# Optimization experiments

Measured on AMD Instinct MI355X. Metric: run time of the kernel, lower is better.

The kernel has to match this reference:

```python
import jax, jax.numpy as jnp
import numpy as np

H, TH, NH, NL, NB = 512, 768, 8, 12, 2
NE, NU, NI, NNZ, K, B = 16000, 2000, 4000, 40000, 10, 64
MD = H // 2
GAMA = 0.1


def _prelu(x, a):
    return jnp.where(x >= 0, x, a * x)


def _spmm(r, c, v, X, n):
    # sparse [n, m] @ X: gather X rows by col index, scale, segment-sum by row.
    return jax.ops.segment_sum(v[:, None] * X[c], r, num_segments=n)


def _forward(systemid, adj_row, adj_col, itemid_set,
             token_embeds, adj_val, node_embeds, user_embedding,
             token_proj_w, token_proj_b, trans_w, trans_b, trans_t_w, trans_t_b,
             meta_w1, meta_b1, meta_w2, meta_b2, sim_w1, sim_w2,
             p1_w1, p1_b1, p1_w2, p1_b2, p2_w, p2_b, prelu_a):
    tok = token_embeds @ token_proj_w + token_proj_b               # [B, H]
    # grouped mean over rows sharing the same system id (vectorized segment-mean)
    same = (systemid[:, None] == systemid[None, :]).astype(tok.dtype)
    group_mean = (same @ tok) / same.sum(1, keepdims=True)         # [B, H]
    filt = _prelu(group_mean @ trans_w + trans_b, prelu_a) * group_mean
    h = jax.nn.relu(filt @ meta_w1 + meta_b1)
    mapping = (h @ meta_w2 + meta_b2).reshape(B, H, H)             # per-sample hypernet weights
    enhanced = jnp.einsum('bh,bhk->bk', user_embedding[systemid], mapping)
    all_tok = user_embedding.at[systemid].set(enhanced)            # [NU, H]
    tok_edge = jnp.zeros_like(user_embedding).at[systemid].set(group_mean)
    # similarity between (enhanced) user/token reps and item reps
    u_rep = all_tok @ sim_w1
    i_rep = node_embeds[itemid_set] @ sim_w2
    u_n = u_rep / jnp.maximum(jnp.linalg.norm(u_rep, axis=1, keepdims=True), 1e-12)
    i_n = i_rep / jnp.maximum(jnp.linalg.norm(i_rep, axis=1, keepdims=True), 1e-12)
    sim = jax.nn.sigmoid(u_n @ i_n.T)                              # [NU, NI]
    tv, ti = jax.lax.top_k(sim, K)
    # combined sparse adjacency = original COO + per-user top-k added edges
    rows = jnp.concatenate([adj_row, jnp.repeat(jnp.arange(NU), K)])
    cols = jnp.concatenate([adj_col, itemid_set[ti].reshape(-1)])
    vals = jnp.concatenate([adj_val, tv.reshape(-1)])
    v_u = vals / jax.ops.segment_sum(vals, rows, num_segments=NU)[rows]   # row-normalized user->item
    v_i = vals / jax.ops.segment_sum(vals, cols, num_segments=NE)[cols]   # row-normalized item->user
    # LightGCN-style 2-layer propagation with multiplicative token gating
    user_tok = _prelu(tok_edge @ trans_t_w + trans_t_b, prelu_a) * tok_edge
    u0, i0 = all_tok, node_embeds
    Ai0 = _spmm(rows, cols, v_u, i0, NU)
    u1 = Ai0 + Ai0 * user_tok
    Att = _spmm(cols, rows, v_i, user_tok, NE)
    i1 = _spmm(cols, rows, v_i, u0, NE) + Att * i0
    Ai1 = _spmm(rows, cols, v_u, i1, NU)
    u2 = Ai1 + Ai1 * user_tok
    i2 = _spmm(cols, rows, v_i, u1, NE) + Att * i1
    user_final = (u0 + u1 + u2) / 3.0
    item_final = (i0 + i1 + i2) / 3.0
    # reconstruction loss vs dense adjacency restricted to item columns
    inv = jnp.full((NE,), -1, jnp.int32).at[itemid_set].set(jnp.arange(NI, dtype=jnp.int32))
    icol = inv[adj_col]
    valid = (icol >= 0).astype(sim.dtype)
    dense = jnp.zeros((NU, NI), sim.dtype).at[adj_row, jnp.maximum(icol, 0)].add(adj_val * valid)
    loss = GAMA * jnp.mean((sim - dense) ** 2)
    # prefix-prompt projection from per-batch system embeddings
    sys_final = user_final[systemid][:, None, :]                   # [B, 1, H]
    p1 = jax.nn.relu(sys_final @ p1_w1 + p1_b1) @ p1_w2 + p1_b2 + sys_final
    p2 = p1 @ p2_w + p2_b
    prompt = p2.reshape(B, 1, NL, NB, NH, H // NH).transpose(2, 3, 0, 4, 1, 5)
    return prompt, item_final, loss


def setup_inputs():
    ks = jax.random.split(jax.random.key(0), 20)
    rng = np.random.default_rng(0)
    s = 0.02
    itemid_set = jnp.asarray(np.sort(rng.choice(NE, NI, replace=False)).astype(np.int32))
    user_embedding = (s * jax.random.normal(ks[4], (NU, H), jnp.float32)).at[0].set(0.0)
    return {
        'systemid': jax.random.randint(ks[0], (B,), 0, NU),
        'adj_row': jax.random.randint(ks[1], (NNZ,), 0, NU),
        'adj_col': jax.random.randint(ks[2], (NNZ,), 0, NE),
        'itemid_set': itemid_set,
        'token_embeds': jax.random.normal(ks[3], (B, TH), jnp.float32),
        'adj_val': jnp.ones((NNZ,), jnp.float32),
        'node_embeds': s * jax.random.normal(ks[5], (NE, H), jnp.float32),
        'user_embedding': user_embedding,
        'token_proj_w': s * jax.random.normal(ks[6], (TH, H), jnp.float32),
        'token_proj_b': jnp.zeros((H,), jnp.float32),
        'trans_w': s * jax.random.normal(ks[7], (H, H), jnp.float32),
        'trans_b': jnp.zeros((H,), jnp.float32),
        'trans_t_w': s * jax.random.normal(ks[8], (H, H), jnp.float32),
        'trans_t_b': jnp.zeros((H,), jnp.float32),
        'meta_w1': s * jax.random.normal(ks[9], (H, MD), jnp.float32),
        'meta_b1': jnp.zeros((MD,), jnp.float32),
        'meta_w2': s * jax.random.normal(ks[10], (MD, H * H), jnp.float32),
        'meta_b2': jnp.zeros((H * H,), jnp.float32),
        'sim_w1': jax.random.normal(ks[11], (H, H), jnp.float32),
        'sim_w2': jax.random.normal(ks[12], (H, H), jnp.float32),
        'p1_w1': s * jax.random.normal(ks[13], (H, MD), jnp.float32),
        'p1_b1': jnp.zeros((MD,), jnp.float32),
        'p1_w2': s * jax.random.normal(ks[14], (MD, H), jnp.float32),
        'p1_b2': jnp.zeros((H,), jnp.float32),
        'p2_w': s * jax.random.normal(ks[15], (H, NL * NB * H), jnp.float32),
        'p2_b': jnp.zeros((NL * NB * H,), jnp.float32),
        'prelu_a': jnp.array(0.25, jnp.float32),
    }


def reference(systemid, adj_row, adj_col, itemid_set, token_embeds, adj_val,
              node_embeds, user_embedding, token_proj_w, token_proj_b,
              trans_w, trans_b, trans_t_w, trans_t_b,
              meta_w1, meta_b1, meta_w2, meta_b2, sim_w1, sim_w2,
              p1_w1, p1_b1, p1_w2, p1_b2, p2_w, p2_b, prelu_a):
    return _forward(systemid, adj_row, adj_col, itemid_set, token_embeds, adj_val,
                    node_embeds, user_embedding, token_proj_w, token_proj_b,
                    trans_w, trans_b, trans_t_w, trans_t_b,
                    meta_w1, meta_b1, meta_w2, meta_b2, sim_w1, sim_w2,
                    p1_w1, p1_b1, p1_w2, p1_b2, p2_w, p2_b, prelu_a)
```

## Files before the change

### kernel.cpp

```cpp
#include <hip/hip_runtime.h>

#define H     512
#define THD   768
#define MDIM  256
#define NE    16000
#define NU    2000
#define NI    4000
#define NNZ   40000
#define KTOP  10
#define NBATCH 64
#define NEDGE 60000
#define GAMA  0.1f
#define P2N   12288
#define PROMPT_N 786432
#define NLOSSB 2048

__device__ __forceinline__ float sigmoidf(float x){ return 1.0f/(1.0f+expf(-x)); }
__device__ __forceinline__ float4 f4z(){ return make_float4(0.f,0.f,0.f,0.f); }

__device__ __forceinline__ void gll16(const float* g, float* l){
  __builtin_amdgcn_global_load_lds(
      (const __attribute__((address_space(1))) void*)g,
      (__attribute__((address_space(3))) void*)l, 16, 0, 0);
}

__global__ void k_tok(const float* __restrict__ A, const float* __restrict__ W,
                      const float* __restrict__ bias, float* __restrict__ C){
  int b=blockIdx.x, c=blockIdx.y*256+threadIdx.x;
  const float* a=A+b*THD; float s=bias[c];
  for(int k=0;k<THD;k++) s+=a[k]*W[k*H+c];
  C[b*H+c]=s;
}

__global__ void k_gm(const int* __restrict__ sysid, const float* __restrict__ tok,
                     float* __restrict__ gm){
  int b=blockIdx.x, c=blockIdx.y*256+threadIdx.x;
  int sid=sysid[b]; float s=0.f, cnt=0.f;
  for(int j=0;j<NBATCH;j++){ if(sysid[j]==sid){ s+=tok[j*H+c]; cnt+=1.f; } }
  gm[b*H+c]=s/cnt;
}

__global__ __launch_bounds__(512) void k_front(const int* __restrict__ sysid,
        const float* __restrict__ gm,
        const float* __restrict__ trans_w, const float* __restrict__ trans_b,
        const float* __restrict__ mw1, const float* __restrict__ mb1,
        const float* __restrict__ ue, const float* __restrict__ mb2,
        const float* __restrict__ trt_w, const float* __restrict__ trt_b,
        const float* __restrict__ pa,
        float* __restrict__ hh, float* __restrict__ ueT, float* __restrict__ enh,
        float* __restrict__ usertok){
  __shared__ float fl[512];
  __shared__ float hp[512];
  int b=blockIdx.x, t=threadIdx.x, which=blockIdx.y;
  if(which==0){
    const float* g=gm+b*H;
    float s=trans_b[t];
    for(int k=0;k<H;k++) s+=g[k]*trans_w[k*H+t];
    float al=pa[0]; float pr=(s>=0.f)? s : al*s;
    fl[t]=pr*g[t];
    __syncthreads();
    int m=t&255, half=t>>8;
    float s2=0.f; int k0=half*256;
    for(int k=0;k<256;k++) s2+=fl[k0+k]*mw1[(k0+k)*MDIM+m];
    hp[t]=s2;
    __syncthreads();
    if(t<256) hh[b*MDIM+t]=fmaxf(hp[t]+hp[t+256]+mb1[t],0.f);
  } else if(which==1){
    const float* u=ue+(size_t)sysid[b]*H;
    float v=u[t];
    ueT[t*64+b]=v;
    float s=0.f;
    for(int h=0;h<H;h++) s+=u[h]*mb2[(size_t)h*H+t];
    enh[b*H+t]=s;
  } else {
    const float* a=gm+b*H; float s=trt_b[t];
    for(int k=0;k<H;k++) s+=a[k]*trt_w[k*H+t];
    float al=pa[0]; float pr=(s>=0.f)? s : al*s;
    usertok[(size_t)sysid[b]*H+t]=pr*gm[b*H+t];
  }
}

#define HCH 8
__global__ __launch_bounds__(128) void k_big(const float* __restrict__ hh,
        const float* __restrict__ ueT, const float* __restrict__ w2,
        float* __restrict__ partials){
  __shared__ float a_lds[2][HCH][64];
  __shared__ float w_lds[2][HCH][256];
  int m=blockIdx.x;
  int kt=blockIdx.y&1, hs=blockIdx.y>>1;
  int k0=kt*256;
  int hbase=hs*256;
  int t=threadIdx.x;
  int kg=t&15, bg=t>>4;
  const float* w2m = w2 + (size_t)m*(size_t)(H*H);

  float4 acc[8][4];
  #pragma unroll
  for(int r=0;r<8;r++){
    #pragma unroll
    for(int c=0;c<4;c++) acc[r][c]=f4z();
  }

  #define STAGE(buf,hc) do{                                             \
    int h0=hbase+(hc)*HCH;                                              \
    gll16(ueT + (size_t)(h0+(t>>4))*64 + (t&15)*4,                      \
          &a_lds[buf][t>>4][(t&15)*4]);                                 \
    _Pragma("unroll")                                                   \
    for(int j=0;j<4;j++){                                               \
      int i=t+j*128;                                                    \
      gll16(w2m + (size_t)(h0+(i>>6))*H + k0 + (i&63)*4,                \
            &w_lds[buf][i>>6][(i&63)*4]);                               \
    }                                                                   \
  }while(0)

  STAGE(0,0);
  int cur=0;
  for(int hc=0;hc<32;hc++){
    __syncthreads();
    if(hc<31) STAGE(cur^1,hc+1);
    #pragma unroll
    for(int hl=0;hl<HCH;hl++){
      float4 aL=*(const float4*)&a_lds[cur][hl][bg*4];
      float4 aH=*(const float4*)&a_lds[cur][hl][32+bg*4];
      float4 w0=*(const float4*)&w_lds[cur][hl][kg*4];
      float4 w1=*(const float4*)&w_lds[cur][hl][64+kg*4];
      float4 w2v=*(const float4*)&w_lds[cur][hl][128+kg*4];
      float4 w3=*(const float4*)&w_lds[cur][hl][192+kg*4];
      #define FMA4(ac,av,wv) ac.x+=(av)*wv.x; ac.y+=(av)*wv.y; ac.z+=(av)*wv.z; ac.w+=(av)*wv.w;
      #define ROWC(r,av) FMA4(acc[r][0],av,w0) FMA4(acc[r][1],av,w1) FMA4(acc[r][2],av,w2v) FMA4(acc[r][3],av,w3)
      ROWC(0,aL.x) ROWC(1,aL.y) ROWC(2,aL.z) ROWC(3,aL.w)
      ROWC(4,aH.x) ROWC(5,aH.y) ROWC(6,aH.z) ROWC(7,aH.w)
      #undef ROWC
      #undef FMA4
    }
    cur^=1;
  }
  int slice=hs*256+m;
  #pragma unroll
  for(int r=0;r<8;r++){
    int br=(r<4)? (bg*4+r) : (32+bg*4+(r-4));
    float hv=hh[br*MDIM+m];
    float* p=partials+((size_t)slice*NBATCH+br)*H+k0+kg*4;
    *(float4*)(p)    =make_float4(acc[r][0].x*hv,acc[r][0].y*hv,acc[r][0].z*hv,acc[r][0].w*hv);
    *(float4*)(p+64) =make_float4(acc[r][1].x*hv,acc[r][1].y*hv,acc[r][1].z*hv,acc[r][1].w*hv);
    *(float4*)(p+128)=make_float4(acc[r][2].x*hv,acc[r][2].y*hv,acc[r][2].z*hv,acc[r][2].w*hv);
    *(float4*)(p+192)=make_float4(acc[r][3].x*hv,acc[r][3].y*hv,acc[r][3].z*hv,acc[r][3].w*hv);
  }
  #undef STAGE
}

__global__ void k_red1(const float* __restrict__ partials, float* __restrict__ partial2){
  int idx=blockIdx.x*256+threadIdx.x;
  int g=idx>>15, col=idx&32767;
  const float* p=partials+(size_t)g*16*32768+col;
  float s=0.f;
  #pragma unroll
  for(int m=0;m<16;m++) s+=p[(size_t)m*32768];
  partial2[idx]=s;
}
__global__ void k_red2s(const int* __restrict__ sysid, const float* __restrict__ partial2,
                        const float* __restrict__ enh, float* __restrict__ alltok){
  int idx=blockIdx.x*256+threadIdx.x;
  int b=idx>>9, k=idx&511;
  float s=enh[idx];
  #pragma unroll
  for(int g=0;g<32;g++) s+=partial2[(size_t)g*32768+idx];
  alltok[(size_t)sysid[b]*H+k]=s;
}

template<int EPI, bool NT, bool AIDX>
__device__ __forceinline__ void gemm_body(float (*As)[68], float (*Bs)[68],
        const float* __restrict__ A, const float* __restrict__ Bm,
        const float* __restrict__ bias, const int* __restrict__ aidx,
        float* __restrict__ C, int M, int N, int K, int bx, int by){
  int n0=bx*64, m0=by*64;
  int t=threadIdx.x;
  int tn=t&15, tm=t>>4;
  float4 pa[2], pb[2];
  #pragma unroll
  for(int i=0;i<2;i++){
    int idx=t+i*256; int r=idx>>3, q=idx&7;
    int grow=m0+r;
    pa[i]=f4z();
    if(grow<M){
      const float* arow=A+(size_t)(AIDX? aidx[grow]:grow)*K;
      pa[i]=*(const float4*)(arow+q*4);
    }
  }
  #pragma unroll
  for(int i=0;i<2;i++){
    if(!NT){
      int idx=t+i*256; int r=idx>>4, q=idx&15;
      pb[i]=*(const float4*)(Bm+(size_t)r*N+n0+q*4);
    } else {
      int idx=t+i*256; int r=idx>>3, q=idx&7;
      int gn=n0+r;
      pb[i]=f4z();
      if(gn<N) pb[i]=*(const float4*)(Bm+(size_t)gn*K+q*4);
    }
  }
  float acc[4][4]={};
  for(int kt=0;kt<K;kt+=32){
    __syncthreads();
    #pragma unroll
    for(int i=0;i<2;i++){
      int idx=t+i*256; int r=idx>>3, q=idx&7;
      As[q*4+0][r]=pa[i].x; As[q*4+1][r]=pa[i].y; As[q*4+2][r]=pa[i].z; As[q*4+3][r]=pa[i].w;
    }
    #pragma unroll
    for(int i=0;i<2;i++){
      if(!NT){
        int idx=t+i*256; int r=idx>>4, q=idx&15;
        *(float4*)&Bs[r][q*4]=pb[i];
      } else {
        int idx=t+i*256; int r=idx>>3, q=idx&7;
        Bs[q*4+0][r]=pb[i].x; Bs[q*4+1][r]=pb[i].y; Bs[q*4+2][r]=pb[i].z; Bs[q*4+3][r]=pb[i].w;
      }
    }
    __syncthreads();
    if(kt+32<K){
      #pragma unroll
      for(int i=0;i<2;i++){
        int idx=t+i*256; int r=idx>>3, q=idx&7;
        int grow=m0+r;
        pa[i]=f4z();
        if(grow<M){
          const float* arow=A+(size_t)(AIDX? aidx[grow]:grow)*K;
          pa[i]=*(const float4*)(arow+kt+32+q*4);
        }
      }
      #pragma unroll
      for(int i=0;i<2;i++){
        if(!NT){
          int idx=t+i*256; int r=idx>>4, q=idx&15;
          pb[i]=*(const float4*)(Bm+(size_t)(kt+32+r)*N+n0+q*4);
        } else {
          int idx=t+i*256; int r=idx>>3, q=idx&7;
          int gn=n0+r;
          pb[i]=f4z();
          if(gn<N) pb[i]=*(const float4*)(Bm+(size_t)gn*K+kt+32+q*4);
        }
      }
    }
    #pragma unroll 8
    for(int k=0;k<32;k++){
      float4 a4=*(const float4*)&As[k][tm*4];
      float4 b4=*(const float4*)&Bs[k][tn*4];
      acc[0][0]+=a4.x*b4.x; acc[0][1]+=a4.x*b4.y; acc[0][2]+=a4.x*b4.z; acc[0][3]+=a4.x*b4.w;
      acc[1][0]+=a4.y*b4.x; acc[1][1]+=a4.y*b4.y; acc[1][2]+=a4.y*b4.z; acc[1][3]+=a4.y*b4.w;
      acc[2][0]+=a4.z*b4.x; acc[2][1]+=a4.z*b4.y; acc[2][2]+=a4.z*b4.z; acc[2][3]+=a4.z*b4.w;
      acc[3][0]+=a4.w*b4.x; acc[3][1]+=a4.w*b4.y; acc[3][2]+=a4.w*b4.z; acc[3][3]+=a4.w*b4.w;
    }
  }
  #pragma unroll
  for(int bi=0;bi<4;bi++){
    int row=m0+tm*4+bi; if(row>=M) continue;
    #pragma unroll
    for(int ki=0;ki<4;ki++){
      int col=n0+tn*4+ki; if(col>=N) continue;
      float v=acc[bi][ki];
      if(EPI==0){ if(bias) v+=bias[col]; }
      else { v=sigmoidf(v); }
      C[(size_t)row*N+col]=v;
    }
  }
}

template<int EPI, bool NT, bool AIDX>
__global__ __launch_bounds__(256) void k_gemm(const float* __restrict__ A,
        const float* __restrict__ Bm, const float* __restrict__ bias,
        const int* __restrict__ aidx, float* __restrict__ C, int M, int N, int K){
  __shared__ float As[32][68];
  __shared__ float Bs[32][68];
  gemm_body<EPI,NT,AIDX>(As,Bs,A,Bm,bias,aidx,C,M,N,K,blockIdx.x,blockIdx.y);
}

__global__ __launch_bounds__(256) void k_gemm_ui(const float* __restrict__ alltok,
        const float* __restrict__ node_emb, const float* __restrict__ sw1,
        const float* __restrict__ sw2, const int* __restrict__ itemid,
        float* __restrict__ urep, float* __restrict__ irep){
  __shared__ float As[32][68];
  __shared__ float Bs[32][68];
  if(blockIdx.y<32)
    gemm_body<0,false,false>(As,Bs,alltok,sw1,nullptr,nullptr,urep,NU,H,H,blockIdx.x,blockIdx.y);
  else
    gemm_body<0,false,true >(As,Bs,node_emb,sw2,nullptr,itemid,irep,NI,H,H,blockIdx.x,blockIdx.y-32);
}

__global__ __launch_bounds__(512) void k_gemm_sim(const float* __restrict__ A,
        const float* __restrict__ Bm, float* __restrict__ C, int M, int N){
  __shared__ float As[32][132];
  __shared__ float Bs[32][260];
  int n0=blockIdx.x*256, m0=blockIdx.y*128;
  int t=threadIdx.x;
  int tn=t&31, tm=t>>5;
  float4 pa[2], pb[4];
  #pragma unroll
  for(int i=0;i<2;i++){
    int idx=t+i*512; int r=idx>>3, q=idx&7;
    pa[i]=f4z();
    if(m0+r<M) pa[i]=*(const float4*)(A+(size_t)(m0+r)*H+q*4);
  }
  #pragma unroll
  for(int i=0;i<4;i++){
    int idx=t+i*512; int r=idx>>3, q=idx&7;
    pb[i]=f4z();
    if(n0+r<N) pb[i]=*(const float4*)(Bm+(size_t)(n0+r)*H+q*4);
  }
  float4 acc[8][2];
  #pragma unroll
  for(int r=0;r<8;r++){ acc[r][0]=f4z(); acc[r][1]=f4z(); }
  for(int kt=0;kt<H;kt+=32){
    __syncthreads();
    #pragma unroll
    for(int i=0;i<2;i++){
      int idx=t+i*512; int r=idx>>3, q=idx&7;
      As[q*4+0][r]=pa[i].x; As[q*4+1][r]=pa[i].y; As[q*4+2][r]=pa[i].z; As[q*4+3][r]=pa[i].w;
    }
    #pragma unroll
    for(int i=0;i<4;i++){
      int idx=t+i*512; int r=idx>>3, q=idx&7;
      Bs[q*4+0][r]=pb[i].x; Bs[q*4+1][r]=pb[i].y; Bs[q*4+2][r]=pb[i].z; Bs[q*4+3][r]=pb[i].w;
    }
    __syncthreads();
    if(kt+32<H){
      #pragma unroll
      for(int i=0;i<2;i++){
        int idx=t+i*512; int r=idx>>3, q=idx&7;
        pa[i]=f4z();
        if(m0+r<M) pa[i]=*(const float4*)(A+(size_t)(m0+r)*H+kt+32+q*4);
      }
      #pragma unroll
      for(int i=0;i<4;i++){
        int idx=t+i*512; int r=idx>>3, q=idx&7;
        pb[i]=f4z();
        if(n0+r<N) pb[i]=*(const float4*)(Bm+(size_t)(n0+r)*H+kt+32+q*4);
      }
    }
    #pragma unroll 8
    for(int k=0;k<32;k++){
      float4 a0=*(const float4*)&As[k][tm*4];
      float4 a1=*(const float4*)&As[k][64+tm*4];
      float4 b0=*(const float4*)&Bs[k][tn*4];
      float4 b1=*(const float4*)&Bs[k][128+tn*4];
      #define FMA4(ac,av,bv) ac.x+=(av)*bv.x; ac.y+=(av)*bv.y; ac.z+=(av)*bv.z; ac.w+=(av)*bv.w;
      #define ROW(r,av) FMA4(acc[r][0],av,b0) FMA4(acc[r][1],av,b1)
      ROW(0,a0.x) ROW(1,a0.y) ROW(2,a0.z) ROW(3,a0.w)
      ROW(4,a1.x) ROW(5,a1.y) ROW(6,a1.z) ROW(7,a1.w)
      #undef ROW
      #undef FMA4
    }
  }
  #pragma unroll
  for(int r=0;r<8;r++){
    int row=m0+((r<4)? (tm*4+r) : (64+tm*4+(r-4)));
    if(row>=M) continue;
    #pragma unroll
    for(int c=0;c<2;c++){
      int col0=n0+c*128+tn*4;
      float vv[4]={acc[r][c].x,acc[r][c].y,acc[r][c].z,acc[r][c].w};
      #pragma unroll
      for(int j=0;j<4;j++){
        int col=col0+j;
        if(col<N) C[(size_t)row*N+col]=sigmoidf(vv[j]);
      }
    }
  }
}

__global__ __launch_bounds__(256) void k_rownorm2(float* __restrict__ U, float* __restrict__ I){
  int r=blockIdx.x, t=threadIdx.x;
  float* X=(r<NU)? U+(size_t)r*H : I+(size_t)(r-NU)*H;
  float v1=X[t], v2=X[t+256];
  float ss=v1*v1+v2*v2;
  for(int o=32;o;o>>=1) ss+=__shfl_xor(ss,o);
  __shared__ float red[4];
  if((t&63)==0) red[t>>6]=ss;
  __syncthreads();
  float tot=red[0]+red[1]+red[2]+red[3];
  float nrm=fmaxf(sqrtf(tot),1e-12f);
  X[t]=v1/nrm; X[t+256]=v2/nrm;
}

__global__ __launch_bounds__(256) void k_topk(const float* __restrict__ sim,
        float* __restrict__ tv, int* __restrict__ ti){
  __shared__ float rv[4];
  __shared__ int   ri[4];
  int u=blockIdx.x, t=threadIdx.x;
  float v[16];
  #pragma unroll
  for(int j=0;j<16;j++){
    int gi=t+j*256;
    v[j]=(gi<NI)? sim[(size_t)u*NI+gi] : -1e30f;
  }
  for(int k=0;k<KTOP;k++){
    float bv=-1e30f; int bi=1<<30;
    #pragma unroll
    for(int j=0;j<16;j++){
      int gi=t+j*256;
      if(v[j]>bv){ bv=v[j]; bi=gi; }
    }
    #pragma unroll
    for(int o=32;o;o>>=1){
      float ov=__shfl_xor(bv,o); int oi=__shfl_xor(bi,o);
      if(ov>bv || (ov==bv && oi<bi)){ bv=ov; bi=oi; }
    }
    if((t&63)==0){ rv[t>>6]=bv; ri[t>>6]=bi; }
    __syncthreads();
    float fv=rv[0]; int fi=ri[0];
    #pragma unroll
    for(int w=1;w<4;w++){
      float ov=rv[w]; int oi=ri[w];
      if(ov>fv || (ov==fv && oi<fi)){ fv=ov; fi=oi; }
    }
    if(t==0){ tv[u*KTOP+k]=fv; ti[u*KTOP+k]=fi; }
    int jj=fi>>8, tt=fi&255;
    #pragma unroll
    for(int j=0;j<16;j++) if(tt==t && j==jj) v[j]=-1e30f;
    __syncthreads();
  }
}

__global__ void k_edges(const int* __restrict__ adj_row, const int* __restrict__ adj_col,
        const float* __restrict__ adj_val, const int* __restrict__ itemid,
        const float* __restrict__ tv, const int* __restrict__ ti,
        int* __restrict__ rows, int* __restrict__ cols, float* __restrict__ vals,
        float* __restrict__ seg_r, float* __restrict__ seg_c,
        int* __restrict__ row_cnt, int* __restrict__ col_cnt, int* __restrict__ inv){
  int e=blockIdx.x*256+threadIdx.x; if(e>=NEDGE) return;
  if(e<NI) inv[itemid[e]]=e;
  int r,c; float v;
  if(e<NNZ){ r=adj_row[e]; c=adj_col[e]; v=adj_val[e]; }
  else { int x=e-NNZ; int u=x/KTOP; r=u; c=itemid[ti[x]]; v=tv[x]; }
  rows[e]=r; cols[e]=c; vals[e]=v;
  atomicAdd(&seg_r[r],v); atomicAdd(&seg_c[c],v);
  atomicAdd(&row_cnt[r],1); atomicAdd(&col_cnt[c],1);
}

__global__ __launch_bounds__(1024) void k_scan(const int* __restrict__ rc, int* __restrict__ rp,
        const int* __restrict__ cc, int* __restrict__ cp){
  const int* cnt; int* ptr; int n;
  if(blockIdx.x==0){ cnt=rc; ptr=rp; n=NU; } else { cnt=cc; ptr=cp; n=NE; }
  int t=threadIdx.x;
  int chunk=(n+1023)>>10;
  int base=t*chunk;
  int s=0;
  for(int i=0;i<chunk;i++){ int j=base+i; if(j<n) s+=cnt[j]; }
  __shared__ int buf[1024];
  buf[t]=s; __syncthreads();
  for(int off=1;off<1024;off<<=1){
    int y=(t>=off)? buf[t-off]:0;
    __syncthreads();
    buf[t]+=y;
    __syncthreads();
  }
  int run=buf[t]-s;
  for(int i=0;i<chunk;i++){ int j=base+i; if(j<n){ ptr[j]=run; run+=cnt[j]; } }
  if(t==1023) ptr[n]=buf[1023];
}

__global__ void k_fill(const int* __restrict__ rows, const int* __restrict__ cols,
        const float* __restrict__ vals,
        const int* __restrict__ row_ptr, const int* __restrict__ col_ptr,
        const float* __restrict__ seg_r, const float* __restrict__ seg_c,
        int* __restrict__ fr, int* __restrict__ fc,
        int* __restrict__ ebr, int* __restrict__ ebc,
        float* __restrict__ v_u, float* __restrict__ v_i,
        const int* __restrict__ inv, float* __restrict__ dense){
  int e=blockIdx.x*256+threadIdx.x; if(e>=NEDGE) return;
  int r=rows[e], c=cols[e];
  ebr[row_ptr[r]+atomicAdd(&fr[r],1)]=e;
  ebc[col_ptr[c]+atomicAdd(&fc[c],1)]=e;
  v_u[e]=vals[e]/seg_r[r];
  v_i[e]=vals[e]/seg_c[c];
  if(e<NNZ){
    int ic=inv[c];
    if(ic>=0) atomicAdd(&dense[(size_t)r*NI+ic],vals[e]);
  }
}

__device__ __forceinline__ void spmm_u_body(int u, const int* __restrict__ row_ptr,
        const int* __restrict__ ebr, const int* __restrict__ cols,
        const float* __restrict__ v_u, const float* __restrict__ X,
        const float* __restrict__ usertok, float* __restrict__ out,
        int* sc, float* sv, float (*red)[512]){
  int t=threadIdx.x, w=t>>6, l=t&63;
  int s=row_ptr[u], n=row_ptr[u+1]-s;
  float4 a0=f4z(), a1=f4z();
  for(int base=0;base<n;base+=128){
    int cnt=min(n-base,128);
    if(t<cnt){ int e=ebr[s+base+t]; sc[t]=cols[e]; sv[t]=v_u[e]; }
    __syncthreads();
    for(int j=w;j<cnt;j+=4){
      float v=sv[j];
      const float4* xr=(const float4*)(X+(size_t)sc[j]*H);
      float4 x0=xr[l], x1=xr[l+64];
      a0.x+=v*x0.x; a0.y+=v*x0.y; a0.z+=v*x0.z; a0.w+=v*x0.w;
      a1.x+=v*x1.x; a1.y+=v*x1.y; a1.z+=v*x1.z; a1.w+=v*x1.w;
    }
    __syncthreads();
  }
  if(w>0){ *(float4*)&red[w-1][l*4]=a0; *(float4*)&red[w-1][l*4+256]=a1; }
  __syncthreads();
  if(w==0){
    #pragma unroll
    for(int ww=0;ww<3;ww++){
      float4 r0=*(const float4*)&red[ww][l*4], r1=*(const float4*)&red[ww][l*4+256];
      a0.x+=r0.x; a0.y+=r0.y; a0.z+=r0.z; a0.w+=r0.w;
      a1.x+=r1.x; a1.y+=r1.y; a1.z+=r1.z; a1.w+=r1.w;
    }
    const float4* ut=(const float4*)(usertok+(size_t)u*H);
    float4 u0=ut[l], u1=ut[l+64];
    float4* o=(float4*)(out+(size_t)u*H);
    o[l]   =make_float4(a0.x+a0.x*u0.x, a0.y+a0.y*u0.y, a0.z+a0.z*u0.z, a0.w+a0.w*u0.w);
    o[l+64]=make_float4(a1.x+a1.x*u1.x, a1.y+a1.y*u1.y, a1.z+a1.z*u1.z, a1.w+a1.w*u1.w);
  }
}

__device__ __forceinline__ void spmm_i1_body(int ib, const int* __restrict__ col_ptr,
        const int* __restrict__ ebc, const int* __restrict__ rows,
        const float* __restrict__ v_i, const float* __restrict__ alltok,
        const float* __restrict__ usertok, const float* __restrict__ i0,
        float* __restrict__ Att, float* __restrict__ i1){
  int i=ib*4+(threadIdx.x>>6);
  int l=threadIdx.x&63;
  int s=col_ptr[i], e1=col_ptr[i+1];
  float4 aA0=f4z(),aA1=f4z(),aU0=f4z(),aU1=f4z();
  for(int j=s;j<e1;j++){
    int e=ebc[j]; float v=v_i[e]; int r=rows[e];
    const float4* ur=(const float4*)(usertok+(size_t)r*H);
    const float4* ar=(const float4*)(alltok+(size_t)r*H);
    float4 u0=ur[l],u1v=ur[l+64],A0=ar[l],A1=ar[l+64];
    aA0.x+=v*u0.x; aA0.y+=v*u0.y; aA0.z+=v*u0.z; aA0.w+=v*u0.w;
    aA1.x+=v*u1v.x; aA1.y+=v*u1v.y; aA1.z+=v*u1v.z; aA1.w+=v*u1v.w;
    aU0.x+=v*A0.x; aU0.y+=v*A0.y; aU0.z+=v*A0.z; aU0.w+=v*A0.w;
    aU1.x+=v*A1.x; aU1.y+=v*A1.y; aU1.z+=v*A1.z; aU1.w+=v*A1.w;
  }
  size_t o=(size_t)i*128;
  const float4* z=(const float4*)i0;
  float4 z0=z[o+l], z1=z[o+l+64];
  ((float4*)Att)[o+l]   =aA0;
  ((float4*)Att)[o+l+64]=aA1;
  ((float4*)i1)[o+l]   =make_float4(aU0.x+aA0.x*z0.x, aU0.y+aA0.y*z0.y, aU0.z+aA0.z*z0.z, aU0.w+aA0.w*z0.w);
  ((float4*)i1)[o+l+64]=make_float4(aU1.x+aA1.x*z1.x, aU1.y+aA1.y*z1.y, aU1.z+aA1.z*z1.z, aU1.w+aA1.w*z1.w);
}

__device__ __forceinline__ void spmm_i2_body(int ib, const int* __restrict__ col_ptr,
        const int* __restrict__ ebc, const int* __restrict__ rows,
        const float* __restrict__ v_i, const float* __restrict__ u1,
        const float* __restrict__ Att, const float* __restrict__ i1,
        const float* __restrict__ i0, float* __restrict__ item_out){
  int i=ib*4+(threadIdx.x>>6);
  int l=threadIdx.x&63;
  int s=col_ptr[i], e1=col_ptr[i+1];
  float4 a0=f4z(), a1=f4z();
  for(int j=s;j<e1;j++){
    int e=ebc[j]; float v=v_i[e];
    const float4* ur=(const float4*)(u1+(size_t)rows[e]*H);
    float4 x0=ur[l], x1=ur[l+64];
    a0.x+=v*x0.x; a0.y+=v*x0.y; a0.z+=v*x0.z; a0.w+=v*x0.w;
    a1.x+=v*x1.x; a1.y+=v*x1.y; a1.z+=v*x1.z; a1.w+=v*x1.w;
  }
  size_t o=(size_t)i*128;
  float4 A0=((const float4*)Att)[o+l], A1=((const float4*)Att)[o+l+64];
  float4 I0=((const float4*)i1)[o+l],  I1=((const float4*)i1)[o+l+64];
  float4 Z0=((const float4*)i0)[o+l],  Z1=((const float4*)i0)[o+l+64];
  float4 r0=make_float4((Z0.x+I0.x+a0.x+A0.x*I0.x)/3.f,(Z0.y+I0.y+a0.y+A0.y*I0.y)/3.f,
                        (Z0.z+I0.z+a0.z+A0.z*I0.z)/3.f,(Z0.w+I0.w+a0.w+A0.w*I0.w)/3.f);
  float4 r1=make_float4((Z1.x+I1.x+a1.x+A1.x*I1.x)/3.f,(Z1.y+I1.y+a1.y+A1.y*I1.y)/3.f,
                        (Z1.z+I1.z+a1.z+A1.z*I1.z)/3.f,(Z1.w+I1.w+a1.w+A1.w*I1.w)/3.f);
  ((float4*)item_out)[o+l]=r0;
  ((float4*)item_out)[o+l+64]=r1;
}

__device__ __forceinline__ void loss_body(int lb, const float* __restrict__ sim,
        const float* __restrict__ dense, float* __restrict__ acc, float* red){
  int t=threadIdx.x;
  size_t n4=(size_t)NU*NI/4;
  float s=0.f;
  for(size_t i=(size_t)lb*256+t; i<n4; i+=(size_t)NLOSSB*256){
    float4 a=((const float4*)sim)[i], d=((const float4*)dense)[i];
    float dx=a.x-d.x, dy=a.y-d.y, dz=a.z-d.z, dw=a.w-d.w;
    s+=dx*dx+dy*dy+dz*dz+dw*dw;
  }
  red[t]=s; __syncthreads();
  for(int o=128;o;o>>=1){ if(t<o) red[t]+=red[t+o]; __syncthreads(); }
  if(t==0) atomicAdd(acc,red[0]);
}

__global__ __launch_bounds__(256) void k_stage1(const int* __restrict__ row_ptr,
        const int* __restrict__ ebr, const int* __restrict__ colsA,
        const float* __restrict__ v_u, const float* __restrict__ node_emb,
        const float* __restrict__ usertok, float* __restrict__ u1,
        const int* __restrict__ col_ptr, const int* __restrict__ ebc,
        const int* __restrict__ rowsA, const float* __restrict__ v_i,
        const float* __restrict__ alltok, float* __restrict__ Att, float* __restrict__ i1,
        const float* __restrict__ sim, const float* __restrict__ dense,
        float* __restrict__ loss_acc){
  __shared__ int   sc[128];
  __shared__ float sv[128];
  __shared__ float red[3][512];
  int bid=blockIdx.x;
  if(bid<NU)              spmm_u_body(bid,row_ptr,ebr,colsA,v_u,node_emb,usertok,u1,sc,sv,red);
  else if(bid<NU+NE/4)    spmm_i1_body(bid-NU,col_ptr,ebc,rowsA,v_i,alltok,usertok,node_emb,Att,i1);
  else                    loss_body(bid-(NU+NE/4),sim,dense,loss_acc,(float*)red);
}

__global__ __launch_bounds__(256) void k_stage2(const int* __restrict__ row_ptr,
        const int* __restrict__ ebr, const int* __restrict__ colsA,
        const float* __restrict__ v_u, const float* __restrict__ i1,
        const float* __restrict__ usertok, float* __restrict__ u2,
        const int* __restrict__ col_ptr, const int* __restrict__ ebc,
        const int* __restrict__ rowsA, const float* __restrict__ v_i,
        const float* __restrict__ u1, const float* __restrict__ Att,
        const float* __restrict__ node_emb, float* __restrict__ item_out){
  __shared__ int   sc[128];
  __shared__ float sv[128];
  __shared__ float red[3][512];
  int bid=blockIdx.x;
  if(bid<NU) spmm_u_body(bid,row_ptr,ebr,colsA,v_u,i1,usertok,u2,sc,sv,red);
  else       spmm_i2_body(bid-NU,col_ptr,ebc,rowsA,v_i,u1,Att,i1,node_emb,item_out);
}

__global__ void k_loss_write(const float* __restrict__ acc, float* __restrict__ out){
  out[0]=GAMA*(acc[0]/(float)((size_t)NU*NI));
}

__global__ __launch_bounds__(512) void k_sysq_p1(const int* __restrict__ sysid,
        const float* __restrict__ u0, const float* __restrict__ u1, const float* __restrict__ u2,
        const float* __restrict__ p1w1, const float* __restrict__ p1b1,
        const float* __restrict__ p1w2, const float* __restrict__ p1b2,
        float* __restrict__ p1buf){
  __shared__ float sf[512];
  __shared__ float hp[512];
  __shared__ float qv[256];
  int b=blockIdx.x, t=threadIdx.x;
  size_t o=(size_t)sysid[b]*H+t;
  float sfv=(u0[o]+u1[o]+u2[o])/3.0f;
  sf[t]=sfv;
  __syncthreads();
  int m=t&255, half=t>>8;
  float s=0.f; int k0=half*256;
  for(int k=0;k<256;k++) s+=sf[k0+k]*p1w1[(k0+k)*MDIM+m];
  hp[t]=s;
  __syncthreads();
  if(t<256) qv[t]=fmaxf(hp[t]+hp[t+256]+p1b1[t],0.f);
  __syncthreads();
  float s2=p1b2[t];
  for(int k=0;k<256;k++) s2+=qv[k]*p1w2[k*H+t];
  p1buf[b*H+t]=s2+sf[t];
}

__global__ void k_perm(const float* __restrict__ p2, float* __restrict__ out){
  int idx=blockIdx.x*256+threadIdx.x;
  int x=idx&511;
  int b=(idx>>9)&63;
  int c=idx>>15;
  out[idx]=p2[(size_t)b*P2N+c*512+x];
}

extern "C" void kernel_launch(void* const* d_in, const int* in_sizes, int n_in,
                              void* d_out, int out_size, void* d_ws, size_t ws_size,
                              hipStream_t stream){
  const int*   sysid   =(const int*)  d_in[0];
  const int*   adj_row =(const int*)  d_in[1];
  const int*   adj_col =(const int*)  d_in[2];
  const int*   itemid  =(const int*)  d_in[3];
  const float* tok_emb =(const float*)d_in[4];
  const float* adj_val =(const float*)d_in[5];
  const float* node_emb=(const float*)d_in[6];
  const float* user_emb=(const float*)d_in[7];
  const float* tp_w    =(const float*)d_in[8];
  const float* tp_b    =(const float*)d_in[9];
  const float* trans_w =(const float*)d_in[10];
  const float* trans_b =(const float*)d_in[11];
  const float* trt_w   =(const float*)d_in[12];
  const float* trt_b   =(const float*)d_in[13];
  const float* mw1     =(const float*)d_in[14];
  const float* mb1     =(const float*)d_in[15];
  const float* mw2     =(const float*)d_in[16];
  const float* mb2     =(const float*)d_in[17];
  const float* sw1     =(const float*)d_in[18];
  const float* sw2     =(const float*)d_in[19];
  const float* p1w1    =(const float*)d_in[20];
  const float* p1b1    =(const float*)d_in[21];
  const float* p1w2    =(const float*)d_in[22];
  const float* p1b2    =(const float*)d_in[23];
  const float* p2w     =(const float*)d_in[24];
  const float* p2b     =(const float*)d_in[25];
  const float* pa      =(const float*)d_in[26];

  float* out_prompt=(float*)d_out;
  float* out_item  =out_prompt+PROMPT_N;
  float* out_loss  =out_item+(size_t)NE*H;

  char* ws=(char*)d_ws; size_t off=0;
  auto A=[&](size_t bytes)->char*{ char* p=ws+off; off+=(bytes+255)&~(size_t)255; return p; };
  float* tok     =(float*)A((size_t)NBATCH*H*4);
  float* gm      =(float*)A((size_t)NBATCH*H*4);
  float* hh      =(float*)A((size_t)NBATCH*MDIM*4);
  float* ueT     =(float*)A((size_t)H*NBATCH*4);
  float* enh     =(float*)A((size_t)NBATCH*H*4);
  float* irep    =(float*)A((size_t)NI*H*4);
  float* alltok  =(float*)A((size_t)NU*H*4);
  float* urep    =(float*)A((size_t)NU*H*4);
  float* u1      =(float*)A((size_t)NU*H*4);
  float* u2      =(float*)A((size_t)NU*H*4);
  float* partials=(float*)A((size_t)512*NBATCH*H*4);
  float* partial2=(float*)A((size_t)32*32768*4);
  float* sim     =(float*)A((size_t)NU*NI*4);
  float* dense   =(float*)A((size_t)NU*NI*4);
  float* Att     =(float*)A((size_t)NE*H*4);
  float* i1      =(float*)A((size_t)NE*H*4);
  float* tv      =(float*)A((size_t)NU*KTOP*4);
  int*   ti      =(int*)  A((size_t)NU*KTOP*4);
  int*   rowsA   =(int*)  A((size_t)NEDGE*4);
  int*   colsA   =(int*)  A((size_t)NEDGE*4);
  float* valsA   =(float*)A((size_t)NEDGE*4);
  float* v_u     =(float*)A((size_t)NEDGE*4);
  float* v_i     =(float*)A((size_t)NEDGE*4);
  int*   ebr     =(int*)  A((size_t)NEDGE*4);
  int*   ebc     =(int*)  A((size_t)NEDGE*4);
  int*   row_ptr =(int*)  A((size_t)(NU+1)*4);
  int*   col_ptr =(int*)  A((size_t)(NE+1)*4);
  size_t zb_bytes=(size_t)NU*H*4 + (size_t)(NU+NE)*4*3 + 256;
  char*  zb      =A(zb_bytes);
  float* usertok =(float*)zb;
  float* seg_r   =usertok+(size_t)NU*H;
  float* seg_c   =seg_r+NU;
  int*   row_cnt =(int*)(seg_c+NE);
  int*   col_cnt =row_cnt+NU;
  int*   fr      =col_cnt+NE;
  int*   fc      =fr+NU;
  float* loss_acc=(float*)(fc+NE);
  int*   inv     =(int*)  A((size_t)NE*4);
  float* p1buf   =(float*)A((size_t)NBATCH*H*4);
  float* p2buf   =(float*)A((size_t)NBATCH*P2N*4);
  (void)ws_size; (void)n_in; (void)in_sizes; (void)out_size;

  hipMemcpyAsync(alltok,user_emb,(size_t)NU*H*4,hipMemcpyDeviceToDevice,stream);
  hipMemsetAsync(zb,0,zb_bytes,stream);
  hipMemsetAsync(inv,0xFF,(size_t)NE*4,stream);
  hipMemsetAsync(dense,0,(size_t)NU*NI*4,stream);

  k_tok  <<<dim3(NBATCH,2),256,0,stream>>>(tok_emb,tp_w,tp_b,tok);
  k_gm   <<<dim3(NBATCH,2),256,0,stream>>>(sysid,tok,gm);
  k_front<<<dim3(NBATCH,3),512,0,stream>>>(sysid,gm,trans_w,trans_b,mw1,mb1,
                                           user_emb,mb2,trt_w,trt_b,pa,
                                           hh,ueT,enh,usertok);
  k_big  <<<dim3(256,4),128,0,stream>>>(hh,ueT,mw2,partials);
  k_red1 <<<4096,256,0,stream>>>(partials,partial2);
  k_red2s<<<128,256,0,stream>>>(sysid,partial2,enh,alltok);

  k_gemm_ui<<<dim3(8,95),256,0,stream>>>(alltok,node_emb,sw1,sw2,itemid,urep,irep);
  k_rownorm2<<<NU+NI,256,0,stream>>>(urep,irep);
  k_gemm_sim<<<dim3(16,16),512,0,stream>>>(urep,irep,sim,NU,NI);
  k_topk<<<NU,256,0,stream>>>(sim,tv,ti);

  k_edges<<<(NEDGE+255)/256,256,0,stream>>>(adj_row,adj_col,adj_val,itemid,tv,ti,
                                            rowsA,colsA,valsA,seg_r,seg_c,row_cnt,col_cnt,inv);
  k_scan<<<2,1024,0,stream>>>(row_cnt,row_ptr,col_cnt,col_ptr);
  k_fill<<<(NEDGE+255)/256,256,0,stream>>>(rowsA,colsA,valsA,row_ptr,col_ptr,seg_r,seg_c,
                                           fr,fc,ebr,ebc,v_u,v_i,inv,dense);

  k_stage1<<<NU+NE/4+NLOSSB,256,0,stream>>>(row_ptr,ebr,colsA,v_u,node_emb,usertok,u1,
                                            col_ptr,ebc,rowsA,v_i,alltok,Att,i1,
                                            sim,dense,loss_acc);
  k_loss_write<<<1,1,0,stream>>>(loss_acc,out_loss);

  k_stage2<<<NU+NE/4,256,0,stream>>>(row_ptr,ebr,colsA,v_u,i1,usertok,u2,
                                     col_ptr,ebc,rowsA,v_i,u1,Att,node_emb,out_item);

  k_sysq_p1<<<NBATCH,512,0,stream>>>(sysid,alltok,u1,u2,p1w1,p1b1,p1w2,p1b2,p1buf);
  k_gemm<0,false,false><<<dim3(192,1),256,0,stream>>>(p1buf,p2w,p2b,nullptr,p2buf,NBATCH,P2N,H);
  k_perm<<<PROMPT_N/256,256,0,stream>>>(p2buf,out_prompt);
}
```

Baseline: 700.8 us.

## Fuse small kernels: item GEMM into reduction, loss write into stage2, permute into GEMM epilogue

The item-side projection GEMM (irep), which does not depend on the hypernetwork reduction, now runs in the same launch as the first partial-sum reduction so the two can overlap. The user GEMM stays separate after k_red2s. The scalar loss write is folded into an extra block of stage2. The final p2 GEMM writes directly into the permuted prompt layout, which removes the p2buf intermediate and the k_perm kernel. This saves launches and a round trip of about 3 MB, at the cost of scattered (though still 512-contiguous) stores in the GEMM epilogue.

Result: slower. 727.4 us (+3.8%).

```diff
diff --git a/kernel.cpp b/kernel.cpp
--- a/kernel.cpp
+++ b/kernel.cpp
@@ -149,26 +149,7 @@
   #undef STAGE
 }
 
-__global__ void k_red1(const float* __restrict__ partials, float* __restrict__ partial2){
-  int idx=blockIdx.x*256+threadIdx.x;
-  int g=idx>>15, col=idx&32767;
-  const float* p=partials+(size_t)g*16*32768+col;
-  float s=0.f;
-  #pragma unroll
-  for(int m=0;m<16;m++) s+=p[(size_t)m*32768];
-  partial2[idx]=s;
-}
-__global__ void k_red2s(const int* __restrict__ sysid, const float* __restrict__ partial2,
-                        const float* __restrict__ enh, float* __restrict__ alltok){
-  int idx=blockIdx.x*256+threadIdx.x;
-  int b=idx>>9, k=idx&511;
-  float s=enh[idx];
-  #pragma unroll
-  for(int g=0;g<32;g++) s+=partial2[(size_t)g*32768+idx];
-  alltok[(size_t)sysid[b]*H+k]=s;
-}
-
-template<int EPI, bool NT, bool AIDX>
+template<int EPI, bool NT, bool AIDX, bool PERM>
 __device__ __forceinline__ void gemm_body(float (*As)[68], float (*Bs)[68],
         const float* __restrict__ A, const float* __restrict__ Bm,
         const float* __restrict__ bias, const int* __restrict__ aidx,
@@ -261,30 +242,54 @@
       float v=acc[bi][ki];
       if(EPI==0){ if(bias) v+=bias[col]; }
       else { v=sigmoidf(v); }
-      C[(size_t)row*N+col]=v;
-    }
-  }
-}
-
-template<int EPI, bool NT, bool AIDX>
+      if(PERM){
+        size_t oidx=(size_t)(col>>9)*32768 + (size_t)row*512 + (col&511);
+        C[oidx]=v;
+      } else {
+        C[(size_t)row*N+col]=v;
+      }
+    }
+  }
+}
+
+template<int EPI, bool NT, bool AIDX, bool PERM>
 __global__ __launch_bounds__(256) void k_gemm(const float* __restrict__ A,
         const float* __restrict__ Bm, const float* __restrict__ bias,
         const int* __restrict__ aidx, float* __restrict__ C, int M, int N, int K){
   __shared__ float As[32][68];
   __shared__ float Bs[32][68];
-  gemm_body<EPI,NT,AIDX>(As,Bs,A,Bm,bias,aidx,C,M,N,K,blockIdx.x,blockIdx.y);
-}
-
-__global__ __launch_bounds__(256) void k_gemm_ui(const float* __restrict__ alltok,
-        const float* __restrict__ node_emb, const float* __restrict__ sw1,
+  gemm_body<EPI,NT,AIDX,PERM>(As,Bs,A,Bm,bias,aidx,C,M,N,K,blockIdx.x,blockIdx.y);
+}
+
+__global__ __launch_bounds__(256) void k_red1i(const float* __restrict__ partials,
+        float* __restrict__ partial2, const float* __restrict__ node_emb,
         const float* __restrict__ sw2, const int* __restrict__ itemid,
-        float* __restrict__ urep, float* __restrict__ irep){
+        float* __restrict__ irep){
   __shared__ float As[32][68];
   __shared__ float Bs[32][68];
-  if(blockIdx.y<32)
-    gemm_body<0,false,false>(As,Bs,alltok,sw1,nullptr,nullptr,urep,NU,H,H,blockIdx.x,blockIdx.y);
-  else
-    gemm_body<0,false,true >(As,Bs,node_emb,sw2,nullptr,itemid,irep,NI,H,H,blockIdx.x,blockIdx.y-32);
+  int bid=blockIdx.x;
+  if(bid<4096){
+    int idx=bid*256+threadIdx.x;
+    int g=idx>>15, col=idx&32767;
+    const float* p=partials+(size_t)g*16*32768+col;
+    float s=0.f;
+    #pragma unroll
+    for(int m=0;m<16;m++) s+=p[(size_t)m*32768];
+    partial2[idx]=s;
+  } else {
+    int b2=bid-4096;
+    gemm_body<0,false,true,false>(As,Bs,node_emb,sw2,nullptr,itemid,irep,NI,H,H,b2&7,b2>>3);
+  }
+}
+
+__global__ void k_red2s(const int* __restrict__ sysid, const float* __restrict__ partial2,
+                        const float* __restrict__ enh, float* __restrict__ alltok){
+  int idx=blockIdx.x*256+threadIdx.x;
+  int b=idx>>9, k=idx&511;
+  float s=enh[idx];
+  #pragma unroll
+  for(int g=0;g<32;g++) s+=partial2[(size_t)g*32768+idx];
+  alltok[(size_t)sysid[b]*H+k]=s;
 }
 
 __global__ __launch_bounds__(512) void k_gemm_sim(const float* __restrict__ A,
@@ -613,17 +618,15 @@
         const int* __restrict__ col_ptr, const int* __restrict__ ebc,
         const int* __restrict__ rowsA, const float* __restrict__ v_i,
         const float* __restrict__ u1, const float* __restrict__ Att,
-        const float* __restrict__ node_emb, float* __restrict__ item_out){
+        const float* __restrict__ node_emb, float* __restrict__ item_out,
+        const float* __restrict__ loss_acc, float* __restrict__ out_loss){
   __shared__ int   sc[128];
   __shared__ float sv[128];
   __shared__ float red[3][512];
   int bid=blockIdx.x;
   if(bid<NU) spmm_u_body(bid,row_ptr,ebr,colsA,v_u,i1,usertok,u2,sc,sv,red);
-  else       spmm_i2_body(bid-NU,col_ptr,ebc,rowsA,v_i,u1,Att,i1,node_emb,item_out);
-}
-
-__global__ void k_loss_write(const float* __restrict__ acc, float* __restrict__ out){
-  out[0]=GAMA*(acc[0]/(float)((size_t)NU*NI));
+  else if(bid<NU+NE/4) spmm_i2_body(bid-NU,col_ptr,ebc,rowsA,v_i,u1,Att,i1,node_emb,item_out);
+  else if(threadIdx.x==0) out_loss[0]=GAMA*(loss_acc[0]/(float)((size_t)NU*NI));
 }
 
 __global__ __launch_bounds__(512) void k_sysq_p1(const int* __restrict__ sysid,
@@ -649,14 +652,6 @@
   float s2=p1b2[t];
   for(int k=0;k<256;k++) s2+=qv[k]*p1w2[k*H+t];
   p1buf[b*H+t]=s2+sf[t];
-}
-
-__global__ void k_perm(const float* __restrict__ p2, float* __restrict__ out){
-  int idx=blockIdx.x*256+threadIdx.x;
-  int x=idx&511;
-  int b=(idx>>9)&63;
-  int c=idx>>15;
-  out[idx]=p2[(size_t)b*P2N+c*512+x];
 }
 
 extern "C" void kernel_launch(void* const* d_in, const int* in_sizes, int n_in,
@@ -735,7 +730,6 @@
   float* loss_acc=(float*)(fc+NE);
   int*   inv     =(int*)  A((size_t)NE*4);
   float* p1buf   =(float*)A((size_t)NBATCH*H*4);
-  float* p2buf   =(float*)A((size_t)NBATCH*P2N*4);
   (void)ws_size; (void)n_in; (void)in_sizes; (void)out_size;
 
   hipMemcpyAsync(alltok,user_emb,(size_t)NU*H*4,hipMemcpyDeviceToDevice,stream);
@@ -749,10 +743,10 @@
                                            user_emb,mb2,trt_w,trt_b,pa,
                                            hh,ueT,enh,usertok);
   k_big  <<<dim3(256,4),128,0,stream>>>(hh,ueT,mw2,partials);
-  k_red1 <<<4096,256,0,stream>>>(partials,partial2);
+  k_red1i<<<4096+504,256,0,stream>>>(partials,partial2,node_emb,sw2,itemid,irep);
   k_red2s<<<128,256,0,stream>>>(sysid,partial2,enh,alltok);
 
-  k_gemm_ui<<<dim3(8,95),256,0,stream>>>(alltok,node_emb,sw1,sw2,itemid,urep,irep);
+  k_gemm<0,false,false,false><<<dim3(8,32),256,0,stream>>>(alltok,sw1,nullptr,nullptr,urep,NU,H,H);
   k_rownorm2<<<NU+NI,256,0,stream>>>(urep,irep);
   k_gemm_sim<<<dim3(16,16),512,0,stream>>>(urep,irep,sim,NU,NI);
   k_topk<<<NU,256,0,stream>>>(sim,tv,ti);
@@ -766,12 +760,11 @@
   k_stage1<<<NU+NE/4+NLOSSB,256,0,stream>>>(row_ptr,ebr,colsA,v_u,node_emb,usertok,u1,
                                             col_ptr,ebc,rowsA,v_i,alltok,Att,i1,
                                             sim,dense,loss_acc);
-  k_loss_write<<<1,1,0,stream>>>(loss_acc,out_loss);
-
-  k_stage2<<<NU+NE/4,256,0,stream>>>(row_ptr,ebr,colsA,v_u,i1,usertok,u2,
-                                     col_ptr,ebc,rowsA,v_i,u1,Att,node_emb,out_item);
+
+  k_stage2<<<NU+NE/4+1,256,0,stream>>>(row_ptr,ebr,colsA,v_u,i1,usertok,u2,
+                                       col_ptr,ebc,rowsA,v_i,u1,Att,node_emb,out_item,
+                                       loss_acc,out_loss);
 
   k_sysq_p1<<<NBATCH,512,0,stream>>>(sysid,alltok,u1,u2,p1w1,p1b1,p1w2,p1b2,p1buf);
-  k_gemm<0,false,false><<<dim3(192,1),256,0,stream>>>(p1buf,p2w,p2b,nullptr,p2buf,NBATCH,P2N,H);
-  k_perm<<<PROMPT_N/256,256,0,stream>>>(p2buf,out_prompt);
-}
+  k_gemm<0,false,false,true><<<dim3(192,1),256,0,stream>>>(p1buf,p2w,p2b,nullptr,out_prompt,NBATCH,P2N,H);
+}
```
